# Performance work log

Hardware: AMD Instinct MI355X
Metric: run time of the kernel (lower is better)

The kernel has to match this reference:

```python
import jax, jax.numpy as jnp
import numpy as np

SEQ_LEN = 2048
N_FFT = 4096   # rfft length n >= seq_len (repo uses next power of two of ~2*seq)
K = 24         # num_eigh
D = 768        # n_embd
BATCH = 1


def _spectral_filters(seq_len: int, k: int) -> jnp.ndarray:
    # Hankel matrix Z[i,j] = 2 / ((i+j)^3 - (i+j)), 1-indexed
    e = np.arange(1, seq_len + 1, dtype=np.float64)
    ipj = e[:, None] + e[None, :]
    Z = 2.0 / (ipj ** 3 - ipj)
    sigma, phi = np.linalg.eigh(Z)
    sigma, phi = sigma[-k:], phi[:, -k:]
    phi = phi * sigma ** 0.25
    return jnp.asarray(phi, dtype=jnp.float32)  # (seq_len, K)


def setup_inputs() -> dict:
    key = jax.random.key(0)
    k1, k2, k3 = jax.random.split(key, 3)
    x = jax.random.normal(k1, (BATCH, SEQ_LEN, D), dtype=jnp.float32)
    M_phi_plus = jax.random.normal(k2, (K, D, D), dtype=jnp.float32) * 0.02
    M_phi_minus = jax.random.normal(k3, (K, D, D), dtype=jnp.float32) * 0.02
    phi = _spectral_filters(SEQ_LEN, K)
    return {"x": x, "phi": phi, "M_phi_plus": M_phi_plus, "M_phi_minus": M_phi_minus}


def _convolve(u, v, n):
    # u: (b, seq, d), v: (seq, K)
    bsz, seq, d = u.shape
    k = v.shape[1]
    # alternating sign sequence (+1, -1, +1, ...)
    sgn = jnp.where(jnp.arange(seq) % 2 == 1, -1.0, 1.0)[None, :, None, None]  # (1,seq,1,1)
    V = jnp.fft.rfft(v.reshape(1, seq, k, 1, 1).astype(jnp.float32), n=n, axis=1)
    u4 = jnp.broadcast_to(u[:, :, None, :], (bsz, seq, k, d))  # (b,seq,K,d)
    U = jnp.stack([u4, u4 * sgn], axis=-1).astype(jnp.float32)  # (b,seq,K,d,2)
    Uf = jnp.fft.rfft(U, n=n, axis=1)
    U_conv = jnp.fft.irfft(V * Uf, n=n, axis=1)[:, :seq]  # (b,seq,K,d,2)
    U_plus = U_conv[..., 0]
    U_minus = U_conv[..., 1] * sgn
    return U_plus, U_minus


def reference(x, phi, M_phi_plus, M_phi_minus):
    U_plus, U_minus = _convolve(x, phi, N_FFT)
    spectral_plus = jnp.einsum('bskd,kde->bse', U_plus, M_phi_plus)
    spectral_minus = jnp.einsum('bskd,kde->bse', U_minus, M_phi_minus)
    return spectral_plus + spectral_minus
```

## Files before the change

kernel.cpp:

```cpp
#include <hip/hip_runtime.h>
#include <hip/hip_bf16.h>
#include <stdint.h>

#define SEQ 2048
#define DDIM 768
#define KF 24
#define NKV 48
#define NZC 8

typedef unsigned short ushort_t;
typedef __attribute__((ext_vector_type(8))) short short8;
typedef __attribute__((ext_vector_type(4))) float f32x4;

typedef __attribute__((address_space(3))) uint32_t lds_u32;
typedef __attribute__((address_space(1))) uint32_t glb_u32;

__device__ __forceinline__ unsigned short f2bf(float f) {
    union { float f; uint32_t u; } v; v.f = f;
    uint32_t u = v.u;
    return (unsigned short)((u + 0x7fff + ((u >> 16) & 1)) >> 16);
}


__global__ void k_pack_x(const float* __restrict__ x, ushort_t* __restrict__ xpk) {
    int b = blockIdx.x;
    int tt = b / 12, ks = b % 12;
    int tid = threadIdx.x;
    ushort_t* dst = xpk + (size_t)b * 8192;
    const float* src = x + (size_t)tt * 128 * DDIM + ks * 64;
#pragma unroll
    for (int p = 0; p < 4; ++p) {
        int s = p * 256 + tid;
        int row = s >> 3, sl = s & 7;
        const float* rp = src + (size_t)row * DDIM + sl * 8;
        float4 a = *(const float4*)rp;
        float4 c = *(const float4*)(rp + 4);
        ushort_t v[8] = {f2bf(a.x), f2bf(a.y), f2bf(a.z), f2bf(a.w),
                         f2bf(c.x), f2bf(c.y), f2bf(c.z), f2bf(c.w)};
        *(uint4*)(dst + row * 64 + ((sl ^ (row & 7)) << 3)) = *(uint4*)v;
    }
}

__global__ void k_pack_M(const float* __restrict__ Mp, const float* __restrict__ Mm,
                         ushort_t* __restrict__ Mpk) {
    __shared__ ushort_t lt[128 * 66];
    int b = blockIdx.x;
    int kv = b / 72; int rem = b % 72; int et = rem / 12, ks = rem % 12;
    const float* src = ((kv < KF) ? Mp + (size_t)kv * DDIM * DDIM
                                  : Mm + (size_t)(kv - KF) * DDIM * DDIM)
                       + (size_t)(ks * 64) * DDIM + et * 128;
    int tid = threadIdx.x;
#pragma unroll
    for (int p = 0; p < 32; ++p) {
        int lin = p * 256 + tid;
        int d = lin >> 7, e = lin & 127;
        lt[e * 66 + d] = f2bf(src[(size_t)d * DDIM + e]);
    }
    __syncthreads();
    ushort_t* dst = Mpk + (size_t)b * 8192;
#pragma unroll
    for (int p = 0; p < 4; ++p) {
        int s = p * 256 + tid; int row = s >> 3, sl = s & 7;
        ushort_t v[8];
#pragma unroll
        for (int j = 0; j < 8; ++j) v[j] = lt[row * 66 + sl * 8 + j];
        *(uint4*)(dst + row * 64 + ((sl ^ (row & 7)) << 3)) = *(uint4*)v;
    }
}

__global__ void k_build_T(const float* __restrict__ phi, ushort_t* __restrict__ Tpk) {
    __shared__ float phiL[256];
    int b = blockIdx.x;
    int kv = b / 17, slot = b % 17;
    int dm = slot - 1;
    int tid = threadIdx.x;
    int tau = 128 * dm - 127 + tid;
    float v = 0.f;
    if (tid < 255 && tau >= 0 && tau < SEQ)
        v = phi[(size_t)tau * KF + kv];
    phiL[tid] = v;
    __syncthreads();
    ushort_t* dst = Tpk + (size_t)b * 2 * 8192;
#pragma unroll
    for (int h = 0; h < 2; ++h) {
#pragma unroll
        for (int p = 0; p < 4; ++p) {
            int s = p * 256 + tid; int row = s >> 3, sl = s & 7;
            ushort_t v8[8];
#pragma unroll
            for (int j = 0; j < 8; ++j) {
                int col = h * 64 + sl * 8 + j;
                v8[j] = f2bf(phiL[row - col + 127]);
            }
            *(uint4*)(dst + h * 8192 + row * 64 + ((sl ^ (row & 7)) << 3)) = *(uint4*)v8;
        }
    }
}


__device__ __forceinline__ void read_frags(const ushort_t* As, const ushort_t* Bs,
                                           int lane, int wm, int wn, int kk,
                                           short8 av[4], short8 bv[4]) {
    int slot = kk * 4 + (lane >> 4);
#pragma unroll
    for (int m = 0; m < 4; ++m) {
        int row = wm * 64 + m * 16 + (lane & 15);
        av[m] = *(const short8*)(As + row * 64 + ((slot ^ (row & 7)) << 3));
    }
#pragma unroll
    for (int n = 0; n < 4; ++n) {
        int row = wn * 64 + n * 16 + (lane & 15);
        bv[n] = *(const short8*)(Bs + row * 64 + ((slot ^ (row & 7)) << 3));
    }
}

__device__ __forceinline__ void mfma16(const short8 av[4], const short8 bv[4], f32x4 acc[4][4]) {
    __builtin_amdgcn_s_setprio(1);
#pragma unroll
    for (int m = 0; m < 4; ++m)
#pragma unroll
        for (int n = 0; n < 4; ++n)
            acc[m][n] = __builtin_amdgcn_mfma_f32_16x16x32_bf16(av[m], bv[n], acc[m][n], 0, 0, 0);
    __builtin_amdgcn_s_setprio(0);
}

__global__ __launch_bounds__(256, 2)
void k_gemm_A(const ushort_t* __restrict__ Mpk, const ushort_t* __restrict__ xpk,
              ushort_t* __restrict__ Apk) {
    __shared__ ushort_t smem[2][2][8192];
    int bid = blockIdx.x;
    int lid = (bid & 7) * 576 + (bid >> 3);
    int kv = lid / 96; int rem = lid % 96; int et = rem / 16, tt = rem % 16;
    const ushort_t* Abase = Mpk + ((size_t)(kv * 6 + et) * 12) * 8192;
    const ushort_t* Bbase = xpk + (size_t)(tt * 12) * 8192;
    int tid = threadIdx.x, lane = tid & 63, wave = tid >> 6;
    int wm = wave >> 1, wn = wave & 1;

    auto stage4 = [&](const ushort_t* src, ushort_t* dst) {
        const char* s = (const char*)src + wave * 4096 + lane * 16;
        char* l = (char*)dst + wave * 4096;
#pragma unroll
        for (int p = 0; p < 4; ++p)
            __builtin_amdgcn_global_load_lds((const glb_u32*)(s + p * 1024),
                                             (lds_u32*)(l + p * 1024), 16, 0, 0);
    };

    f32x4 acc[4][4];
#pragma unroll
    for (int m = 0; m < 4; ++m)
#pragma unroll
        for (int n = 0; n < 4; ++n) acc[m][n] = (f32x4){0.f, 0.f, 0.f, 0.f};

    stage4(Abase, smem[0][0]);
    stage4(Bbase, smem[0][1]);

    for (int s = 0; s < 12; ++s) {
        int c = s & 1;
        bool more = (s + 1 < 12);
        if (more) {
            stage4(Abase + (s + 1) * 8192, smem[c ^ 1][0]);
            asm volatile("s_waitcnt vmcnt(4)" ::: "memory");
        } else {
            asm volatile("s_waitcnt vmcnt(0)" ::: "memory");
        }
        __builtin_amdgcn_s_barrier();
        __builtin_amdgcn_sched_barrier(0);

        const ushort_t* As = smem[c][0];
        const ushort_t* Bs = smem[c][1];
        short8 av[2][4], bv[2][4];
#pragma unroll
        for (int kk = 0; kk < 2; ++kk) {
            int slot = kk * 4 + (lane >> 4);
#pragma unroll
            for (int m = 0; m < 4; ++m) {
                int row = wm * 64 + m * 16 + (lane & 15);
                av[kk][m] = *(const short8*)(As + row * 64 + ((slot ^ (row & 7)) << 3));
            }
#pragma unroll
            for (int n = 0; n < 4; ++n) {
                int row = wn * 64 + n * 16 + (lane & 15);
                bv[kk][n] = *(const short8*)(Bs + row * 64 + ((slot ^ (row & 7)) << 3));
            }
        }
        if (more) stage4(Bbase + (s + 1) * 8192, smem[c ^ 1][1]);

        asm volatile("s_waitcnt lgkmcnt(0)" ::: "memory");
        __builtin_amdgcn_sched_barrier(0);

        __builtin_amdgcn_s_setprio(1);
#pragma unroll
        for (int kk = 0; kk < 2; ++kk)
#pragma unroll
            for (int m = 0; m < 4; ++m)
#pragma unroll
                for (int n = 0; n < 4; ++n)
                    acc[m][n] = __builtin_amdgcn_mfma_f32_16x16x32_bf16(av[kk][m], bv[kk][n], acc[m][n], 0, 0, 0);
        __builtin_amdgcn_s_setprio(0);
        __builtin_amdgcn_s_barrier();
    }

    float fs = (kv >= KF && (lane & 1)) ? -1.f : 1.f;
    ushort_t* sm = &smem[0][0][0];
#pragma unroll
    for (int m = 0; m < 4; ++m) {
        int rb = wm * 64 + m * 16 + ((lane >> 4) << 2);
#pragma unroll
        for (int n = 0; n < 4; ++n) {
            int cb = wn * 64 + n * 16 + (lane & 15);
            int h = cb >> 6, c6 = cb & 63, sl = c6 >> 3, j = c6 & 7;
#pragma unroll
            for (int r = 0; r < 4; ++r) {
                int row = rb + r;
                sm[h * 8192 + row * 64 + ((sl ^ (row & 7)) << 3) + j] = f2bf(fs * acc[m][n][r]);
            }
        }
    }
    __syncthreads();
    uint4* d4 = (uint4*)(Apk + ((size_t)((kv * 6 + et) * 16 + tt) * 2) * 8192);
    const uint4* s4 = (const uint4*)sm;
#pragma unroll
    for (int p = 0; p < 8; ++p) d4[p * 256 + tid] = s4[p * 256 + tid];
}

__global__ __launch_bounds__(256, 2)
void k_gemm_Bv6(const ushort_t* __restrict__ Tpk, const ushort_t* __restrict__ Apk,
                float* __restrict__ outz) {
    __shared__ ushort_t smem[2][2][8192];

    int bid = blockIdx.x;
    int lid = (bid & 7) * 54 + (bid >> 3);
    int et = lid / 72;
    int r = lid % 72;
    int zc = 0;
#pragma unroll
    for (int z = 1; z < 8; ++z) if (r >= z * (17 - z)) zc = z;
    int i1 = 2 * zc + (r - zc * (17 - zc));
    int jlo = zc * 2;

    int tid = threadIdx.x, lane = tid & 63, wave = tid >> 6;
    int wm = wave >> 1, wn = wave & 1;

    f32x4 accp[4][4], accm[4][4];
#pragma unroll
    for (int m = 0; m < 4; ++m)
#pragma unroll
        for (int n = 0; n < 4; ++n) {
            accp[m][n] = (f32x4){0.f, 0.f, 0.f, 0.f};
            accm[m][n] = (f32x4){0.f, 0.f, 0.f, 0.f};
        }

    auto timg = [&](int kv24, int jjs, int h) -> const ushort_t* {
        return Tpk + ((size_t)((kv24 * 17 + (i1 - (jlo + jjs) + 1)) * 2 + h)) * 8192;
    };
    auto aimg = [&](int kv24, int sign, int jjs, int h) -> const ushort_t* {
        return Apk + ((size_t)((((kv24 + KF * sign) * 6 + et) * 16 + (jlo + jjs)) * 2 + h)) * 8192;
    };
    auto stage4 = [&](const ushort_t* src, ushort_t* dst) {
        const char* s = (const char*)src + wave * 4096 + lane * 16;
        char* l = (char*)dst + wave * 4096;
#pragma unroll
        for (int p = 0; p < 4; ++p)
            __builtin_amdgcn_global_load_lds((const glb_u32*)(s + p * 1024),
                                             (lds_u32*)(l + p * 1024), 16, 0, 0);
    };

    stage4(timg(0, 0, 0), smem[0][0]);
    stage4(aimg(0, 0, 0, 0), smem[0][1]);

    for (int kv24 = 0; kv24 < KF; ++kv24) {
#pragma unroll
        for (int rem = 0; rem < 8; ++rem) {
            const int sign = (rem >> 1) & 1, h = rem & 1;
            const int c = h;
            const int nrem = (rem + 1) & 7;
            const int njjs = nrem >> 2, nsign = (nrem >> 1) & 1, nh = nrem & 1;
            int nkv = kv24 + (rem == 7);
            bool more = (nkv < KF);

            if (more) {
                stage4(timg(nkv, njjs, nh), smem[c ^ 1][0]);
                asm volatile("s_waitcnt vmcnt(4)" ::: "memory");
            } else {
                asm volatile("s_waitcnt vmcnt(0)" ::: "memory");
            }
            __builtin_amdgcn_s_barrier();
            __builtin_amdgcn_sched_barrier(0);

            const ushort_t* As = smem[c][0];
            const ushort_t* Bs = smem[c][1];
            short8 av[2][4], bv[2][4];
#pragma unroll
            for (int kk = 0; kk < 2; ++kk) {
                int slot = kk * 4 + (lane >> 4);
#pragma unroll
                for (int m = 0; m < 4; ++m) {
                    int row = wm * 64 + m * 16 + (lane & 15);
                    av[kk][m] = *(const short8*)(As + row * 64 + ((slot ^ (row & 7)) << 3));
                }
#pragma unroll
                for (int n = 0; n < 4; ++n) {
                    int row = wn * 64 + n * 16 + (lane & 15);
                    bv[kk][n] = *(const short8*)(Bs + row * 64 + ((slot ^ (row & 7)) << 3));
                }
            }
            if (more) stage4(aimg(nkv, nsign, njjs, nh), smem[c ^ 1][1]);

            asm volatile("s_waitcnt lgkmcnt(0)" ::: "memory");
            __builtin_amdgcn_sched_barrier(0);

            __builtin_amdgcn_s_setprio(1);
            if (sign == 0) {
#pragma unroll
                for (int kk = 0; kk < 2; ++kk)
#pragma unroll
                    for (int m = 0; m < 4; ++m)
#pragma unroll
                        for (int n = 0; n < 4; ++n)
                            accp[m][n] = __builtin_amdgcn_mfma_f32_16x16x32_bf16(av[kk][m], bv[kk][n], accp[m][n], 0, 0, 0);
            } else {
#pragma unroll
                for (int kk = 0; kk < 2; ++kk)
#pragma unroll
                    for (int m = 0; m < 4; ++m)
#pragma unroll
                        for (int n = 0; n < 4; ++n)
                            accm[m][n] = __builtin_amdgcn_mfma_f32_16x16x32_bf16(av[kk][m], bv[kk][n], accm[m][n], 0, 0, 0);
            }
            __builtin_amdgcn_s_setprio(0);
            __builtin_amdgcn_s_barrier();
        }
    }

    float* dst = outz + ((size_t)zc * SEQ + (size_t)i1 * 128) * DDIM + et * 128;
#pragma unroll
    for (int m = 0; m < 4; ++m) {
        int rb = wm * 64 + m * 16 + ((lane >> 4) << 2);
#pragma unroll
        for (int n = 0; n < 4; ++n) {
            int cb = wn * 64 + n * 16 + (lane & 15);
#pragma unroll
            for (int r4 = 0; r4 < 4; ++r4) {
                float vm = accm[m][n][r4];
                float v = accp[m][n][r4] + ((r4 & 1) ? -vm : vm);
                dst[(size_t)(rb + r4) * DDIM + cb] = v;
            }
        }
    }
}

__global__ void k_reduce(const float* __restrict__ outz, float* __restrict__ out, int n4) {
    int idx = blockIdx.x * blockDim.x + threadIdx.x;
    if (idx < n4) {
        int srow = idx / (DDIM / 4);
        int zmax = srow >> 8;
        if (zmax > NZC - 1) zmax = NZC - 1;
        float4 s = ((const float4*)outz)[idx];
        for (int z = 1; z <= zmax; ++z) {
            float4 t = ((const float4*)(outz + (size_t)z * SEQ * DDIM))[idx];
            s.x += t.x; s.y += t.y; s.z += t.z; s.w += t.w;
        }
        ((float4*)out)[idx] = s;
    }
}

extern "C" void kernel_launch(void* const* d_in, const int* in_sizes, int n_in,
                              void* d_out, int out_size, void* d_ws, size_t ws_size,
                              hipStream_t stream) {
    (void)in_sizes; (void)n_in;
    const float* x   = (const float*)d_in[0];
    const float* phi = (const float*)d_in[1];
    const float* Mp  = (const float*)d_in[2];
    const float* Mm  = (const float*)d_in[3];
    float* out = (float*)d_out;

    char* ws = (char*)d_ws;
    size_t off = 0;
    auto alloc = [&](size_t bytes) { size_t o = off; off += (bytes + 255) & ~(size_t)255; return o; };
    size_t o_xpk = alloc((size_t)16 * 12 * 8192 * 2);
    size_t o_Mpk = alloc((size_t)NKV * 6 * 12 * 8192 * 2);
    size_t o_Tpk = alloc((size_t)KF * 17 * 2 * 8192 * 2);
    size_t o_Apk = alloc((size_t)NKV * 6 * 16 * 2 * 8192 * 2);
    if (off > ws_size) {
        hipMemsetAsync(d_out, 0, (size_t)out_size * 4, stream);
        return;
    }

    ushort_t* xpk = (ushort_t*)(ws + o_xpk);
    ushort_t* Mpk = (ushort_t*)(ws + o_Mpk);
    ushort_t* Tpk = (ushort_t*)(ws + o_Tpk);
    ushort_t* Apk = (ushort_t*)(ws + o_Apk);
    float*   outz = (float*)(ws + o_Mpk);

    k_pack_x<<<16 * 12, 256, 0, stream>>>(x, xpk);
    k_pack_M<<<NKV * 6 * 12, 256, 0, stream>>>(Mp, Mm, Mpk);
    k_build_T<<<KF * 17, 256, 0, stream>>>(phi, Tpk);
    k_gemm_A<<<NKV * 96, 256, 0, stream>>>(Mpk, xpk, Apk);
    k_gemm_Bv6<<<432, 256, 0, stream>>>(Tpk, Apk, outz);
    int n4 = SEQ * DDIM / 4;
    k_reduce<<<(n4 + 255) / 256, 256, 0, stream>>>(outz, out, n4);
}
```

Baseline: 309.8 us.

## Fuse pack kernels into one launch and reuse T tile across sign pair

Merges the x, M and T packing kernels into a single k_prep launch dispatched by block index, removing two kernel launches and the gaps between them. In the second GEMM the loop order is changed so plus and minus signs alternate while the Toeplitz tile stays resident, so T is loaded once per two iterations. The A tiles now get their own double buffer and are prefetched before the barrier. This cuts global-to-LDS traffic for T, but uses more complex vmcnt accounting and a larger shared-memory footprint in the merged prep kernel.

```diff
diff --git a/kernel.cpp b/kernel.cpp
--- a/kernel.cpp
+++ b/kernel.cpp
@@ -22,77 +22,77 @@
 }
 
 
-__global__ void k_pack_x(const float* __restrict__ x, ushort_t* __restrict__ xpk) {
-    int b = blockIdx.x;
-    int tt = b / 12, ks = b % 12;
+__global__ void k_prep(const float* __restrict__ x, const float* __restrict__ Mp,
+                       const float* __restrict__ Mm, const float* __restrict__ phi,
+                       ushort_t* __restrict__ xpk, ushort_t* __restrict__ Mpk,
+                       ushort_t* __restrict__ Tpk) {
+    __shared__ ushort_t lt[128 * 66];
+    __shared__ float phiL[256];
+    int b0 = blockIdx.x;
     int tid = threadIdx.x;
-    ushort_t* dst = xpk + (size_t)b * 8192;
-    const float* src = x + (size_t)tt * 128 * DDIM + ks * 64;
-#pragma unroll
-    for (int p = 0; p < 4; ++p) {
-        int s = p * 256 + tid;
-        int row = s >> 3, sl = s & 7;
-        const float* rp = src + (size_t)row * DDIM + sl * 8;
-        float4 a = *(const float4*)rp;
-        float4 c = *(const float4*)(rp + 4);
-        ushort_t v[8] = {f2bf(a.x), f2bf(a.y), f2bf(a.z), f2bf(a.w),
-                         f2bf(c.x), f2bf(c.y), f2bf(c.z), f2bf(c.w)};
-        *(uint4*)(dst + row * 64 + ((sl ^ (row & 7)) << 3)) = *(uint4*)v;
-    }
-}
-
-__global__ void k_pack_M(const float* __restrict__ Mp, const float* __restrict__ Mm,
-                         ushort_t* __restrict__ Mpk) {
-    __shared__ ushort_t lt[128 * 66];
-    int b = blockIdx.x;
-    int kv = b / 72; int rem = b % 72; int et = rem / 12, ks = rem % 12;
-    const float* src = ((kv < KF) ? Mp + (size_t)kv * DDIM * DDIM
-                                  : Mm + (size_t)(kv - KF) * DDIM * DDIM)
-                       + (size_t)(ks * 64) * DDIM + et * 128;
-    int tid = threadIdx.x;
-#pragma unroll
-    for (int p = 0; p < 32; ++p) {
-        int lin = p * 256 + tid;
-        int d = lin >> 7, e = lin & 127;
-        lt[e * 66 + d] = f2bf(src[(size_t)d * DDIM + e]);
-    }
-    __syncthreads();
-    ushort_t* dst = Mpk + (size_t)b * 8192;
-#pragma unroll
-    for (int p = 0; p < 4; ++p) {
-        int s = p * 256 + tid; int row = s >> 3, sl = s & 7;
-        ushort_t v[8];
-#pragma unroll
-        for (int j = 0; j < 8; ++j) v[j] = lt[row * 66 + sl * 8 + j];
-        *(uint4*)(dst + row * 64 + ((sl ^ (row & 7)) << 3)) = *(uint4*)v;
-    }
-}
-
-__global__ void k_build_T(const float* __restrict__ phi, ushort_t* __restrict__ Tpk) {
-    __shared__ float phiL[256];
-    int b = blockIdx.x;
-    int kv = b / 17, slot = b % 17;
-    int dm = slot - 1;
-    int tid = threadIdx.x;
-    int tau = 128 * dm - 127 + tid;
-    float v = 0.f;
-    if (tid < 255 && tau >= 0 && tau < SEQ)
-        v = phi[(size_t)tau * KF + kv];
-    phiL[tid] = v;
-    __syncthreads();
-    ushort_t* dst = Tpk + (size_t)b * 2 * 8192;
-#pragma unroll
-    for (int h = 0; h < 2; ++h) {
+
+    if (b0 < 192) {
+        int b = b0;
+        int tt = b / 12, ks = b % 12;
+        ushort_t* dst = xpk + (size_t)b * 8192;
+        const float* src = x + (size_t)tt * 128 * DDIM + ks * 64;
+#pragma unroll
+        for (int p = 0; p < 4; ++p) {
+            int s = p * 256 + tid;
+            int row = s >> 3, sl = s & 7;
+            const float* rp = src + (size_t)row * DDIM + sl * 8;
+            float4 a = *(const float4*)rp;
+            float4 c = *(const float4*)(rp + 4);
+            ushort_t v[8] = {f2bf(a.x), f2bf(a.y), f2bf(a.z), f2bf(a.w),
+                             f2bf(c.x), f2bf(c.y), f2bf(c.z), f2bf(c.w)};
+            *(uint4*)(dst + row * 64 + ((sl ^ (row & 7)) << 3)) = *(uint4*)v;
+        }
+    } else if (b0 < 192 + 3456) {
+        int b = b0 - 192;
+        int kv = b / 72; int rem = b % 72; int et = rem / 12, ks = rem % 12;
+        const float* src = ((kv < KF) ? Mp + (size_t)kv * DDIM * DDIM
+                                      : Mm + (size_t)(kv - KF) * DDIM * DDIM)
+                           + (size_t)(ks * 64) * DDIM + et * 128;
+#pragma unroll
+        for (int p = 0; p < 32; ++p) {
+            int lin = p * 256 + tid;
+            int d = lin >> 7, e = lin & 127;
+            lt[e * 66 + d] = f2bf(src[(size_t)d * DDIM + e]);
+        }
+        __syncthreads();
+        ushort_t* dst = Mpk + (size_t)b * 8192;
 #pragma unroll
         for (int p = 0; p < 4; ++p) {
             int s = p * 256 + tid; int row = s >> 3, sl = s & 7;
-            ushort_t v8[8];
-#pragma unroll
-            for (int j = 0; j < 8; ++j) {
-                int col = h * 64 + sl * 8 + j;
-                v8[j] = f2bf(phiL[row - col + 127]);
-            }
-            *(uint4*)(dst + h * 8192 + row * 64 + ((sl ^ (row & 7)) << 3)) = *(uint4*)v8;
+            ushort_t v[8];
+#pragma unroll
+            for (int j = 0; j < 8; ++j) v[j] = lt[row * 66 + sl * 8 + j];
+            *(uint4*)(dst + row * 64 + ((sl ^ (row & 7)) << 3)) = *(uint4*)v;
+        }
+    } else {
+        int b = b0 - (192 + 3456);
+        int kv = b / 17, slot = b % 17;
+        int dm = slot - 1;
+        int tau = 128 * dm - 127 + tid;
+        float v = 0.f;
+        if (tid < 255 && tau >= 0 && tau < SEQ)
+            v = phi[(size_t)tau * KF + kv];
+        phiL[tid] = v;
+        __syncthreads();
+        ushort_t* dst = Tpk + (size_t)b * 2 * 8192;
+#pragma unroll
+        for (int h = 0; h < 2; ++h) {
+#pragma unroll
+            for (int p = 0; p < 4; ++p) {
+                int s = p * 256 + tid; int row = s >> 3, sl = s & 7;
+                ushort_t v8[8];
+#pragma unroll
+                for (int j = 0; j < 8; ++j) {
+                    int col = h * 64 + sl * 8 + j;
+                    v8[j] = f2bf(phiL[row - col + 127]);
+                }
+                *(uint4*)(dst + h * 8192 + row * 64 + ((sl ^ (row & 7)) << 3)) = *(uint4*)v8;
+            }
         }
     }
 }
@@ -112,16 +112,6 @@
         int row = wn * 64 + n * 16 + (lane & 15);
         bv[n] = *(const short8*)(Bs + row * 64 + ((slot ^ (row & 7)) << 3));
     }
-}
-
-__device__ __forceinline__ void mfma16(const short8 av[4], const short8 bv[4], f32x4 acc[4][4]) {
-    __builtin_amdgcn_s_setprio(1);
-#pragma unroll
-    for (int m = 0; m < 4; ++m)
-#pragma unroll
-        for (int n = 0; n < 4; ++n)
-            acc[m][n] = __builtin_amdgcn_mfma_f32_16x16x32_bf16(av[m], bv[n], acc[m][n], 0, 0, 0);
-    __builtin_amdgcn_s_setprio(0);
 }
 
 __global__ __launch_bounds__(256, 2)
@@ -224,9 +214,9 @@
 }
 
 __global__ __launch_bounds__(256, 2)
-void k_gemm_Bv6(const ushort_t* __restrict__ Tpk, const ushort_t* __restrict__ Apk,
+void k_gemm_Bv7(const ushort_t* __restrict__ Tpk, const ushort_t* __restrict__ Apk,
                 float* __restrict__ outz) {
-    __shared__ ushort_t smem[2][2][8192];
+    __shared__ ushort_t smem[4][8192];
 
     int bid = blockIdx.x;
     int lid = (bid & 7) * 54 + (bid >> 3);
@@ -265,30 +255,33 @@
                                              (lds_u32*)(l + p * 1024), 16, 0, 0);
     };
 
-    stage4(timg(0, 0, 0), smem[0][0]);
-    stage4(aimg(0, 0, 0, 0), smem[0][1]);
+    stage4(timg(0, 0, 0), smem[0]);
+    stage4(aimg(0, 0, 0, 0), smem[2]);
 
     for (int kv24 = 0; kv24 < KF; ++kv24) {
 #pragma unroll
         for (int rem = 0; rem < 8; ++rem) {
-            const int sign = (rem >> 1) & 1, h = rem & 1;
-            const int c = h;
+            const int sign = rem & 1;
+            const int tbuf = (rem >> 1) & 1;
+            const int abuf = rem & 1;
             const int nrem = (rem + 1) & 7;
-            const int njjs = nrem >> 2, nsign = (nrem >> 1) & 1, nh = nrem & 1;
+            const int njjs = nrem >> 2, nh = (nrem >> 1) & 1, nsign = nrem & 1;
             int nkv = kv24 + (rem == 7);
             bool more = (nkv < KF);
 
             if (more) {
-                stage4(timg(nkv, njjs, nh), smem[c ^ 1][0]);
-                asm volatile("s_waitcnt vmcnt(4)" ::: "memory");
+                if (sign) stage4(timg(nkv, njjs, nh), smem[tbuf ^ 1]);
+                stage4(aimg(nkv, nsign, njjs, nh), smem[2 + (abuf ^ 1)]);
+                if (sign) { asm volatile("s_waitcnt vmcnt(8)" ::: "memory"); }
+                else      { asm volatile("s_waitcnt vmcnt(4)" ::: "memory"); }
             } else {
                 asm volatile("s_waitcnt vmcnt(0)" ::: "memory");
             }
             __builtin_amdgcn_s_barrier();
             __builtin_amdgcn_sched_barrier(0);
 
-            const ushort_t* As = smem[c][0];
-            const ushort_t* Bs = smem[c][1];
+            const ushort_t* As = smem[tbuf];
+            const ushort_t* Bs = smem[2 + abuf];
             short8 av[2][4], bv[2][4];
 #pragma unroll
             for (int kk = 0; kk < 2; ++kk) {
@@ -304,7 +297,6 @@
                     bv[kk][n] = *(const short8*)(Bs + row * 64 + ((slot ^ (row & 7)) << 3));
                 }
             }
-            if (more) stage4(aimg(nkv, nsign, njjs, nh), smem[c ^ 1][1]);
 
             asm volatile("s_waitcnt lgkmcnt(0)" ::: "memory");
             __builtin_amdgcn_sched_barrier(0);
@@ -392,11 +384,9 @@
     ushort_t* Apk = (ushort_t*)(ws + o_Apk);
     float*   outz = (float*)(ws + o_Mpk);
 
-    k_pack_x<<<16 * 12, 256, 0, stream>>>(x, xpk);
-    k_pack_M<<<NKV * 6 * 12, 256, 0, stream>>>(Mp, Mm, Mpk);
-    k_build_T<<<KF * 17, 256, 0, stream>>>(phi, Tpk);
+    k_prep<<<192 + 3456 + KF * 17, 256, 0, stream>>>(x, Mp, Mm, phi, xpk, Mpk, Tpk);
     k_gemm_A<<<NKV * 96, 256, 0, stream>>>(Mpk, xpk, Apk);
-    k_gemm_Bv6<<<432, 256, 0, stream>>>(Tpk, Apk, outz);
+    k_gemm_Bv7<<<432, 256, 0, stream>>>(Tpk, Apk, outz);
     int n4 = SEQ * DDIM / 4;
     k_reduce<<<(n4 + 255) / 256, 256, 0, stream>>>(outz, out, n4);
 }
```

After: 301.6 us. 2.7% less time.
